# Kernel optimization log

Measured on AMD Instinct MI355X. Metric: run time of the kernel, lower is better.

## Reference

```python
import jax, jax.numpy as jnp
import numpy as np

B, H, W = 1024, 66, 64
N = 62          # EEG channels / graph nodes
TOPK = 62       # hardcoded in Network
NUM_CLASSES = 3


def setup_inputs() -> dict:
    key = jax.random.key(0)
    ks = jax.random.split(key, 17)
    p = lambda i, s: (jax.random.normal(ks[i], s, jnp.float32) * 0.05)
    return {
        "x": jax.random.normal(ks[0], (B, H, W), jnp.float32),
        "conv_w": p(1, (32, 1, 5, 5)), "conv_b": p(2, (32,)),
        "s1_bn_w": p(3, (480, 64)), "s1_bn_b": p(4, (64,)),
        "s1_g_w": p(5, (480, 32)), "s1_g_b": p(6, (32,)),
        "s2_bn_w": p(7, (32, 64)), "s2_bn_b": p(8, (64,)),
        "s2_g_w": p(9, (32, 32)), "s2_g_b": p(10, (32,)),
        "s3_bn_w": p(11, (32, 64)), "s3_bn_b": p(12, (64,)),
        "s3_g_w": p(13, (32, 32)), "s3_g_b": p(14, (32,)),
        "fc_w": p(15, (620, NUM_CLASSES)), "fc_b": p(16, (NUM_CLASSES,)),
    }


def _maxpool_last(x, k):
    # MaxPool over the last dim with kernel=stride=k, VALID (floor) semantics.
    win = (1,) * (x.ndim - 1) + (k,)
    return jax.lax.reduce_window(x, -jnp.inf, jax.lax.max, win, win, "VALID")


def _sogc(x, bn_w, bn_b, g_w, g_b):
    # x: (Bg, N, F). Self-organized graph construction + DenseGCNConv.
    Bg = x.shape[0]
    xa = jnp.tanh(x @ bn_w + bn_b)                     # (Bg, N, bn)
    adj = jax.nn.softmax(jnp.einsum("bnf,bmf->bnm", xa, xa), axis=2)
    # topk mask per row (scatter of ones at top-k column indices)
    _, idx = jax.lax.top_k(adj, TOPK)                  # (Bg, N, k)
    bi = jnp.arange(Bg)[:, None, None]
    ri = jnp.arange(N)[None, :, None]
    mask = jnp.zeros_like(adj).at[bi, ri, idx].set(1.0)
    adj = adj * mask
    # SOGC adds eye, then DenseGCNConv(add_loop=True) overwrites diag with 1
    d = jnp.arange(N)
    adj = adj.at[:, d, d].set(1.0)
    # symmetric degree normalization with clamp(min=1)
    deg_is = jnp.clip(adj.sum(-1), 1.0, None) ** -0.5  # (Bg, N)
    adj = deg_is[:, :, None] * adj * deg_is[:, None, :]
    return jnp.einsum("bnm,bmo->bno", adj, x @ g_w) + g_b


def reference(x, conv_w, conv_b, s1_bn_w, s1_bn_b, s1_g_w, s1_g_b,
              s2_bn_w, s2_bn_b, s2_g_w, s2_g_b,
              s3_bn_w, s3_bn_b, s3_g_w, s3_g_b, fc_w, fc_b):
    b = x.shape[0]
    h = jax.lax.conv_general_dilated(
        x[:, None], conv_w, (1, 1), "VALID",
        dimension_numbers=("NCHW", "OIHW", "NCHW"))
    h = jax.nn.relu(h + conv_b[None, :, None, None])   # (B,32,62,60)
    h = _maxpool_last(h, 4)                            # (B,32,62,15)
    h = h.reshape(b, -1, 480)                          # (B,62,480)
    h = _sogc(h.reshape(-1, N, 480), s1_bn_w, s1_bn_b, s1_g_w, s1_g_b)
    h = _sogc(h.reshape(-1, N, 32), s2_bn_w, s2_bn_b, s2_g_w, s2_g_b)
    h = _sogc(h.reshape(-1, N, 32), s3_bn_w, s3_bn_b, s3_g_w, s3_g_b)
    h = _maxpool_last(h, 3)                            # (B,62,10)
    h = h.reshape(h.shape[0], -1)                      # (B,620) — adapted head
    return h @ fc_w + fc_b                             # (B,3)
```

## Files before the change

### kernel.cpp

```cpp
#include <hip/hip_runtime.h>
#include <math.h>


typedef short bf16x8 __attribute__((ext_vector_type(8)));
typedef float f32x4  __attribute__((ext_vector_type(4)));
typedef float f32x16 __attribute__((ext_vector_type(16)));

__device__ __forceinline__ unsigned short f32_to_bf16_rne(float f) {
    unsigned int u = __builtin_bit_cast(unsigned int, f);
    u += 0x7fffu + ((u >> 16) & 1u);
    return (unsigned short)(u >> 16);
}
__device__ __forceinline__ float bf16_bits_to_f32(unsigned short h) {
    unsigned int u = ((unsigned int)h) << 16;
    return __builtin_bit_cast(float, u);
}
__device__ __forceinline__ float fast_tanh(float v) {
    v = fminf(fmaxf(v, -15.f), 15.f);
    const float ex = __expf(2.f * v);
    return (ex - 1.f) / (ex + 1.f);
}


__global__ __launch_bounds__(256) void prepack_kernel(
    const float* __restrict__ bnw1, const float* __restrict__ gw1,
    const float* __restrict__ cw,
    const float* __restrict__ bnw2, const float* __restrict__ gw2,
    const float* __restrict__ bnw3, const float* __restrict__ gw3,
    unsigned short* __restrict__ wp)
{
    const int idx = blockIdx.x * 256 + threadIdx.x;
    if (idx < 49152) {
        const int kc = idx / 3072, r = idx - kc * 3072;
        const int q = r / 768, r2 = r - q * 768;
        const int col = r2 >> 3, j = r2 & 7;
        float w = 0.f;
        if (kc < 15) {
            const int s = q * 8 + j;
            const int ko = s * 15 + kc;
            w = (col < 64) ? bnw1[ko * 64 + col] : gw1[ko * 32 + (col - 64)];
        }
        wp[idx] = f32_to_bf16_rne(w);
    } else if (idx >= 92160 && idx < 93696) {
        const int e = idx - 92160;
        const int c = e >> 9, l = (e >> 3) & 63, j = e & 7;
        const int ch = l & 31, dio = l >> 5;
        const int di = (c < 2) ? (2 * c + dio) : (4 + dio);
        const float w = (j < 5 && di < 5) ? cw[ch * 25 + di * 5 + j] : 0.f;
        wp[idx] = f32_to_bf16_rne(w);
    } else if (idx >= 94208 && idx < 100352) {
        const int e2 = idx - 94208;
        const int s = e2 / 3072, r = e2 - s * 3072;
        const int col = r >> 5, k = r & 31;
        const float* bnw = s ? bnw3 : bnw2;
        const float* gw  = s ? gw3  : gw2;
        const float w = (col < 64) ? bnw[k * 64 + col] : gw[k * 32 + (col - 64)];
        wp[idx] = f32_to_bf16_rne(w);
    }
}

__global__ __launch_bounds__(256, 4) void mega_kernel(
    const float* __restrict__ x,
    const float* __restrict__ cb,
    const unsigned short* __restrict__ wp,
    const float* __restrict__ bnb1,  const float* __restrict__ gb1,
    const float* __restrict__ bnb2,  const float* __restrict__ gb2,
    const float* __restrict__ bnb3,  const float* __restrict__ gb3,
    const float* __restrict__ fcw,   const float* __restrict__ fcb,
    float* __restrict__ out)
{
    __shared__ __align__(16) char lds[37632];
    unsigned short* xb   = (unsigned short*)lds;
    unsigned short* Xcol = (unsigned short*)(lds + 13056);
    unsigned short* xaH  = (unsigned short*)lds;
    unsigned short* xaL  = xaH + 4608;
    unsigned short* zB   = xaH + 9216;
    unsigned short* P    = xaH + 11520;
    unsigned short* xB   = xaH + 16128;
    float* degis = (float*)(lds + 37376);

    const int b = blockIdx.x;
    const int tid = threadIdx.x;
    const int wv = tid >> 6, ln = tid & 63;

    const float4* xg = (const float4*)(x + (size_t)b * 4224);
    for (int idx = tid; idx < 1056; idx += 256) {
        const float4 v = xg[idx];
        const int row = idx >> 4, c4 = idx & 15;
        short4 s;
        s.x = (short)f32_to_bf16_rne(v.x);
        s.y = (short)f32_to_bf16_rne(v.y);
        s.z = (short)f32_to_bf16_rne(v.z);
        s.w = (short)f32_to_bf16_rne(v.w);
        *(short4*)(xb + row * 96 + c4 * 4) = s;
    }
    for (int idx = tid; idx < 544; idx += 256) {
        const int row = idx >> 3, w = idx & 7;
        ((unsigned int*)(xb + row * 96 + 64))[w] = 0u;
    }
    if (tid < 128) {
        const int row = 66 + (tid >> 5), w = tid & 31;
        ((unsigned int*)(xb + row * 96))[w] = 0u;
    }
    if (tid < 128)
        ((unsigned int*)(Xcol + 62 * 128))[tid] = 0u;
    __syncthreads();

    const int m = ln & 15, rp = (ln >> 4) & 1, dio = ln >> 5;
    const int ch = ln & 31, hi = ln >> 5;
    bf16x8 Wc[3];
    #pragma unroll
    for (int c = 0; c < 3; ++c)
        Wc[c] = *(const bf16x8*)(wp + 92160 + c * 512 + ln * 8);
    const float cbv = cb[ch];

    const int rt = ln & 15, q = ln >> 4;
    f32x4 acc[6];
    #pragma unroll
    for (int nt = 0; nt < 6; ++nt) acc[nt] = (f32x4){0.f, 0.f, 0.f, 0.f};

    for (int pjg = 0; pjg < 4; ++pjg) {
        const int j0 = pjg * 16;
        for (int p = wv; p < 31; p += 4) {
            const int r0 = 2 * p;
            const unsigned short* base = xb + (r0 + rp + dio) * 96 + j0 + m;
            f32x16 a32;
            #pragma unroll
            for (int i = 0; i < 16; ++i) a32[i] = 0.f;
            #pragma unroll
            for (int c = 0; c < 3; ++c) {
                bf16x8 A;
                A[0] = (short)base[c * 192 + 0];
                A[1] = (short)base[c * 192 + 1];
                A[2] = (short)base[c * 192 + 2];
                A[3] = (short)base[c * 192 + 3];
                A[4] = (short)base[c * 192 + 4];
                A[5] = A[0]; A[6] = A[1]; A[7] = A[2];
                a32 = __builtin_amdgcn_mfma_f32_32x32x16_bf16(A, Wc[c], a32, 0, 0, 0);
            }
            #pragma unroll
            for (int i = 0; i < 4; ++i) {
                const int t = 2 * i + hi;
                const int rpo = t >> 2, g = t & 3;
                float v = fmaxf(fmaxf(a32[4 * i], a32[4 * i + 1]),
                                fmaxf(a32[4 * i + 2], a32[4 * i + 3])) + cbv;
                v = fmaxf(v, 0.f);
                if (!(pjg == 3 && g == 3)) {
                    const int row = r0 + rpo;
                    const int tt = ch * 62 + row;
                    const int n = tt >> 5, sf = tt & 31;
                    Xcol[n * 128 + ((g * 32 + sf) ^ ((n & 7) << 3))] =
                        f32_to_bf16_rne(v);
                }
            }
        }
        __syncthreads();
        {
            const int row = wv * 16 + rt;
            #pragma unroll
            for (int g = 0; g < 4; ++g) {
                const int kc = pjg * 4 + g;
                const bf16x8 A = *(const bf16x8*)(
                    Xcol + row * 128 + (((g * 4 + q) ^ (row & 7)) << 3));
                #pragma unroll
                for (int nt = 0; nt < 6; ++nt) {
                    const bf16x8 Bh = *(const bf16x8*)(
                        wp + kc * 3072 + q * 768 + nt * 128 + rt * 8);
                    acc[nt] = __builtin_amdgcn_mfma_f32_16x16x32_bf16(A, Bh, acc[nt], 0, 0, 0);
                }
            }
        }
        __syncthreads();
    }

    {
        const int rq = wv * 4 + q;
        #pragma unroll
        for (int nt = 0; nt < 4; ++nt) {
            const float bb = bnb1[nt * 16 + rt];
            #pragma unroll
            for (int j = 0; j < 4; ++j) {
                const int r = rq * 4 + j;
                float th = fast_tanh(acc[nt][j] + bb);
                if (r >= 62) th = 0.f;
                const unsigned short h = f32_to_bf16_rne(th);
                const unsigned short l = f32_to_bf16_rne(th - bf16_bits_to_f32(h));
                xaH[r * 72 + nt * 16 + rt] = h;
                xaL[r * 72 + nt * 16 + rt] = l;
            }
        }
        #pragma unroll
        for (int nt = 4; nt < 6; ++nt) {
            const int o = (nt - 4) * 16 + rt;
            unsigned short zv[4];
            #pragma unroll
            for (int j = 0; j < 4; ++j) {
                const int r = rq * 4 + j;
                zv[j] = (r < 62) ? f32_to_bf16_rne(acc[nt][j]) : (unsigned short)0;
            }
            *(ushort4*)(zB + o * 72 + rq * 4) =
                make_ushort4(zv[0], zv[1], zv[2], zv[3]);
        }
    }
    __syncthreads();

    const int c16 = ln & 15;
    const unsigned short* wstg = wp + 94208;

    #pragma unroll 1
    for (int st = 0; st < 3; ++st) {
        f32x4 sacc[4];
        #pragma unroll
        for (int t = 0; t < 4; ++t) sacc[t] = (f32x4){0.f, 0.f, 0.f, 0.f};
        const int arow = (wv * 16 + c16) * 72;
        #pragma unroll
        for (int kh = 0; kh < 2; ++kh) {
            const int chh = (kh * 4 + q) * 8;
            const bf16x8 AH = *(const bf16x8*)(xaH + arow + chh);
            const bf16x8 AL = *(const bf16x8*)(xaL + arow + chh);
            #pragma unroll
            for (int t = 0; t < 4; ++t) {
                const bf16x8 BH = *(const bf16x8*)(xaH + (t * 16 + c16) * 72 + chh);
                const bf16x8 BL = *(const bf16x8*)(xaL + (t * 16 + c16) * 72 + chh);
                sacc[t] = __builtin_amdgcn_mfma_f32_16x16x32_bf16(AH, BH, sacc[t], 0, 0, 0);
                sacc[t] = __builtin_amdgcn_mfma_f32_16x16x32_bf16(AH, BL, sacc[t], 0, 0, 0);
                sacc[t] = __builtin_amdgcn_mfma_f32_16x16x32_bf16(AL, BH, sacc[t], 0, 0, 0);
            }
        }
        float e[4][4], dri[4];
        #pragma unroll
        for (int j = 0; j < 4; ++j) {
            const int n = wv * 16 + q * 4 + j;
            const float v0 = sacc[0][j], v1 = sacc[1][j];
            const float v2 = sacc[2][j], v3 = sacc[3][j];
            float mx = fmaxf(fmaxf(v0, v1), v2);
            if (c16 < 14) mx = fmaxf(mx, v3);
            mx = fmaxf(mx, __shfl_xor(mx, 1));
            mx = fmaxf(mx, __shfl_xor(mx, 2));
            mx = fmaxf(mx, __shfl_xor(mx, 4));
            mx = fmaxf(mx, __shfl_xor(mx, 8));
            float e0 = __expf(v0 - mx), e1 = __expf(v1 - mx), e2 = __expf(v2 - mx);
            float e3 = (c16 < 14) ? __expf(v3 - mx) : 0.f;
            float sum = e0 + e1 + e2 + e3;
            sum += __shfl_xor(sum, 1);
            sum += __shfl_xor(sum, 2);
            sum += __shfl_xor(sum, 4);
            sum += __shfl_xor(sum, 8);
            const float inv = 1.f / sum;
            e0 *= inv; e1 *= inv; e2 *= inv; e3 *= inv;
            if (n < 62 && c16 == (n & 15)) {
                const int dt = n >> 4;
                if (dt == 0) e0 = 1.f;
                else if (dt == 1) e1 = 1.f;
                else if (dt == 2) e2 = 1.f;
                else e3 = 1.f;
            }
            float dg = e0 + e1 + e2 + e3;
            dg += __shfl_xor(dg, 1);
            dg += __shfl_xor(dg, 2);
            dg += __shfl_xor(dg, 4);
            dg += __shfl_xor(dg, 8);
            const float d = rsqrtf(fmaxf(dg, 1.f));
            if (c16 == 0) degis[n] = d;
            dri[j] = d;
            e[j][0] = e0; e[j][1] = e1; e[j][2] = e2; e[j][3] = e3;
        }
        __syncthreads();
        {
            const float dm0 = degis[c16],      dm1 = degis[16 + c16];
            const float dm2 = degis[32 + c16], dm3 = degis[48 + c16];
            #pragma unroll
            for (int j = 0; j < 4; ++j) {
                const int n = wv * 16 + q * 4 + j;
                unsigned short* pr = P + n * 72 + c16;
                if (n < 62) {
                    pr[0]  = f32_to_bf16_rne(e[j][0] * dri[j] * dm0);
                    pr[16] = f32_to_bf16_rne(e[j][1] * dri[j] * dm1);
                    pr[32] = f32_to_bf16_rne(e[j][2] * dri[j] * dm2);
                    pr[48] = f32_to_bf16_rne(e[j][3] * dri[j] * dm3);
                } else { pr[0] = 0; pr[16] = 0; pr[32] = 0; pr[48] = 0; }
            }
        }
        __syncthreads();
        {
            f32x4 oa0 = {0.f, 0.f, 0.f, 0.f}, oa1 = {0.f, 0.f, 0.f, 0.f};
            #pragma unroll
            for (int kh = 0; kh < 2; ++kh) {
                const int chh = (kh * 4 + q) * 8;
                const bf16x8 pa = *(const bf16x8*)(P + (wv * 16 + c16) * 72 + chh);
                const bf16x8 z0 = *(const bf16x8*)(zB + c16 * 72 + chh);
                const bf16x8 z1 = *(const bf16x8*)(zB + (16 + c16) * 72 + chh);
                oa0 = __builtin_amdgcn_mfma_f32_16x16x32_bf16(pa, z0, oa0, 0, 0, 0);
                oa1 = __builtin_amdgcn_mfma_f32_16x16x32_bf16(pa, z1, oa1, 0, 0, 0);
            }
            const float* gbp = (st == 0) ? gb1 : (st == 1) ? gb2 : gb3;
            const float g0 = gbp[c16], g1 = gbp[16 + c16];
            #pragma unroll
            for (int j = 0; j < 4; ++j) {
                const int n = wv * 16 + q * 4 + j;
                unsigned short* xr = xB + n * 40 + c16;
                if (n < 62) {
                    xr[0]  = f32_to_bf16_rne(oa0[j] + g0);
                    xr[16] = f32_to_bf16_rne(oa1[j] + g1);
                } else { xr[0] = 0; xr[16] = 0; }
            }
        }
        __syncthreads();
        if (st == 2) break;

        {
            const unsigned short* wsB = wstg + st * 3072;
            const float* bnbp = (st == 0) ? bnb2 : bnb3;
            const bf16x8 ax = *(const bf16x8*)(xB + (wv * 16 + c16) * 40 + q * 8);
            f32x4 sa[6];
            #pragma unroll
            for (int nt = 0; nt < 6; ++nt) {
                const bf16x8 wb = *(const bf16x8*)(wsB + (nt * 16 + c16) * 32 + q * 8);
                f32x4 zz = {0.f, 0.f, 0.f, 0.f};
                sa[nt] = __builtin_amdgcn_mfma_f32_16x16x32_bf16(ax, wb, zz, 0, 0, 0);
            }
            #pragma unroll
            for (int nt = 0; nt < 4; ++nt) {
                const float bb = bnbp[nt * 16 + c16];
                #pragma unroll
                for (int j = 0; j < 4; ++j) {
                    const int n = wv * 16 + q * 4 + j;
                    float th = fast_tanh(sa[nt][j] + bb);
                    if (n >= 62) th = 0.f;
                    const unsigned short h = f32_to_bf16_rne(th);
                    const unsigned short l = f32_to_bf16_rne(th - bf16_bits_to_f32(h));
                    xaH[n * 72 + nt * 16 + c16] = h;
                    xaL[n * 72 + nt * 16 + c16] = l;
                }
            }
            #pragma unroll
            for (int nt = 4; nt < 6; ++nt) {
                const int o = (nt - 4) * 16 + c16;
                unsigned short zv[4];
                #pragma unroll
                for (int j = 0; j < 4; ++j) {
                    const int n = wv * 16 + q * 4 + j;
                    zv[j] = (n < 62) ? f32_to_bf16_rne(sa[nt][j]) : (unsigned short)0;
                }
                *(ushort4*)(zB + o * 72 + wv * 16 + q * 4) =
                    make_ushort4(zv[0], zv[1], zv[2], zv[3]);
            }
        }
        __syncthreads();
    }

    float a0 = 0.f, a1 = 0.f, a2 = 0.f;
    for (int t = tid; t < 620; t += 256) {
        const int n = t / 10, tt = t - (t / 10) * 10;
        const unsigned short* pr = xB + n * 40 + tt * 3;
        const float p = fmaxf(fmaxf(bf16_bits_to_f32(pr[0]), bf16_bits_to_f32(pr[1])),
                              bf16_bits_to_f32(pr[2]));
        const float* fw = fcw + t * 3;
        a0 = fmaf(p, fw[0], a0);
        a1 = fmaf(p, fw[1], a1);
        a2 = fmaf(p, fw[2], a2);
    }
    #pragma unroll
    for (int off = 32; off; off >>= 1) {
        a0 += __shfl_down(a0, off);
        a1 += __shfl_down(a1, off);
        a2 += __shfl_down(a2, off);
    }
    float* red = degis;
    if (ln == 0) { red[wv * 3 + 0] = a0; red[wv * 3 + 1] = a1; red[wv * 3 + 2] = a2; }
    __syncthreads();
    if (tid == 0) {
        out[b * 3 + 0] = red[0] + red[3] + red[6] + red[9]  + fcb[0];
        out[b * 3 + 1] = red[1] + red[4] + red[7] + red[10] + fcb[1];
        out[b * 3 + 2] = red[2] + red[5] + red[8] + red[11] + fcb[2];
    }
}

extern "C" void kernel_launch(void* const* d_in, const int* in_sizes, int n_in,
                              void* d_out, int out_size, void* d_ws, size_t ws_size,
                              hipStream_t stream) {
    const float* x     = (const float*)d_in[0];
    const float* convw = (const float*)d_in[1];
    const float* convb = (const float*)d_in[2];
    const float* bnw1  = (const float*)d_in[3];
    const float* bnb1  = (const float*)d_in[4];
    const float* gw1   = (const float*)d_in[5];
    const float* gb1   = (const float*)d_in[6];
    const float* bnw2  = (const float*)d_in[7];
    const float* bnb2  = (const float*)d_in[8];
    const float* gw2   = (const float*)d_in[9];
    const float* gb2   = (const float*)d_in[10];
    const float* bnw3  = (const float*)d_in[11];
    const float* bnb3  = (const float*)d_in[12];
    const float* gw3   = (const float*)d_in[13];
    const float* gb3   = (const float*)d_in[14];
    const float* fcw   = (const float*)d_in[15];
    const float* fcb   = (const float*)d_in[16];

    unsigned short* wp = (unsigned short*)d_ws;

    prepack_kernel<<<392, 256, 0, stream>>>(bnw1, gw1, convw, bnw2, gw2,
                                            bnw3, gw3, wp);
    mega_kernel<<<1024, 256, 0, stream>>>(x, convb, wp, bnb1, gb1,
                                          bnb2, gb2, bnb3, gb3,
                                          fcw, fcb, (float*)d_out);
}
```

Before: 87.26 us.

## Switch all MFMA paths from bf16 to fp16 and drop split-precision adjacency GEMM

```diff
diff --git a/kernel.cpp b/kernel.cpp
--- a/kernel.cpp
+++ b/kernel.cpp
@@ -2,18 +2,17 @@
 #include <math.h>
 
 
-typedef short bf16x8 __attribute__((ext_vector_type(8)));
-typedef float f32x4  __attribute__((ext_vector_type(4)));
-typedef float f32x16 __attribute__((ext_vector_type(16)));
-
-__device__ __forceinline__ unsigned short f32_to_bf16_rne(float f) {
-    unsigned int u = __builtin_bit_cast(unsigned int, f);
-    u += 0x7fffu + ((u >> 16) & 1u);
-    return (unsigned short)(u >> 16);
-}
-__device__ __forceinline__ float bf16_bits_to_f32(unsigned short h) {
-    unsigned int u = ((unsigned int)h) << 16;
-    return __builtin_bit_cast(float, u);
+typedef _Float16 f16x8 __attribute__((ext_vector_type(8)));
+typedef short    s16x8 __attribute__((ext_vector_type(8)));
+typedef float    f32x4  __attribute__((ext_vector_type(4)));
+typedef float    f32x16 __attribute__((ext_vector_type(16)));
+
+__device__ __forceinline__ unsigned short f32_to_f16u(float f) {
+    const _Float16 h = (_Float16)f;
+    return __builtin_bit_cast(unsigned short, h);
+}
+__device__ __forceinline__ float f16u_to_f32(unsigned short u) {
+    return (float)__builtin_bit_cast(_Float16, u);
 }
 __device__ __forceinline__ float fast_tanh(float v) {
     v = fminf(fmaxf(v, -15.f), 15.f);
@@ -40,14 +39,14 @@
             const int ko = s * 15 + kc;
             w = (col < 64) ? bnw1[ko * 64 + col] : gw1[ko * 32 + (col - 64)];
         }
-        wp[idx] = f32_to_bf16_rne(w);
+        wp[idx] = f32_to_f16u(w);
     } else if (idx >= 92160 && idx < 93696) {
         const int e = idx - 92160;
         const int c = e >> 9, l = (e >> 3) & 63, j = e & 7;
         const int ch = l & 31, dio = l >> 5;
         const int di = (c < 2) ? (2 * c + dio) : (4 + dio);
         const float w = (j < 5 && di < 5) ? cw[ch * 25 + di * 5 + j] : 0.f;
-        wp[idx] = f32_to_bf16_rne(w);
+        wp[idx] = f32_to_f16u(w);
     } else if (idx >= 94208 && idx < 100352) {
         const int e2 = idx - 94208;
         const int s = e2 / 3072, r = e2 - s * 3072;
@@ -55,7 +54,7 @@
         const float* bnw = s ? bnw3 : bnw2;
         const float* gw  = s ? gw3  : gw2;
         const float w = (col < 64) ? bnw[k * 64 + col] : gw[k * 32 + (col - 64)];
-        wp[idx] = f32_to_bf16_rne(w);
+        wp[idx] = f32_to_f16u(w);
     }
 }
 
@@ -69,15 +68,14 @@
     const float* __restrict__ fcw,   const float* __restrict__ fcb,
     float* __restrict__ out)
 {
-    __shared__ __align__(16) char lds[37632];
+    __shared__ __align__(16) char lds[28416];
     unsigned short* xb   = (unsigned short*)lds;
-    unsigned short* Xcol = (unsigned short*)(lds + 13056);
+    unsigned short* Xcol = (unsigned short*)(lds + 10880);
     unsigned short* xaH  = (unsigned short*)lds;
-    unsigned short* xaL  = xaH + 4608;
-    unsigned short* zB   = xaH + 9216;
-    unsigned short* P    = xaH + 11520;
-    unsigned short* xB   = xaH + 16128;
-    float* degis = (float*)(lds + 37376);
+    unsigned short* zB   = xaH + 4608;
+    unsigned short* P    = xaH + 6912;
+    unsigned short* xB   = xaH + 11520;
+    float* degis = (float*)(lds + 28160);
 
     const int b = blockIdx.x;
     const int tid = threadIdx.x;
@@ -88,19 +86,19 @@
         const float4 v = xg[idx];
         const int row = idx >> 4, c4 = idx & 15;
         short4 s;
-        s.x = (short)f32_to_bf16_rne(v.x);
-        s.y = (short)f32_to_bf16_rne(v.y);
-        s.z = (short)f32_to_bf16_rne(v.z);
-        s.w = (short)f32_to_bf16_rne(v.w);
-        *(short4*)(xb + row * 96 + c4 * 4) = s;
+        s.x = (short)f32_to_f16u(v.x);
+        s.y = (short)f32_to_f16u(v.y);
+        s.z = (short)f32_to_f16u(v.z);
+        s.w = (short)f32_to_f16u(v.w);
+        *(short4*)(xb + row * 80 + c4 * 4) = s;
     }
     for (int idx = tid; idx < 544; idx += 256) {
         const int row = idx >> 3, w = idx & 7;
-        ((unsigned int*)(xb + row * 96 + 64))[w] = 0u;
-    }
-    if (tid < 128) {
+        ((unsigned int*)(xb + row * 80 + 64))[w] = 0u;
+    }
+    if (tid < 64) {
         const int row = 66 + (tid >> 5), w = tid & 31;
-        ((unsigned int*)(xb + row * 96))[w] = 0u;
+        ((unsigned int*)(xb + row * 80))[w] = 0u;
     }
     if (tid < 128)
         ((unsigned int*)(Xcol + 62 * 128))[tid] = 0u;
@@ -108,11 +106,12 @@
 
     const int m = ln & 15, rp = (ln >> 4) & 1, dio = ln >> 5;
     const int ch = ln & 31, hi = ln >> 5;
-    bf16x8 Wc[3];
+    f16x8 Wc[3];
     #pragma unroll
     for (int c = 0; c < 3; ++c)
-        Wc[c] = *(const bf16x8*)(wp + 92160 + c * 512 + ln * 8);
+        Wc[c] = *(const f16x8*)(wp + 92160 + c * 512 + ln * 8);
     const float cbv = cb[ch];
+    const f32x16 z16 = {};
 
     const int rt = ln & 15, q = ln >> 4;
     f32x4 acc[6];
@@ -123,20 +122,20 @@
         const int j0 = pjg * 16;
         for (int p = wv; p < 31; p += 4) {
             const int r0 = 2 * p;
-            const unsigned short* base = xb + (r0 + rp + dio) * 96 + j0 + m;
+            const unsigned short* base = xb + (r0 + rp + dio) * 80 + j0 + m;
             f32x16 a32;
             #pragma unroll
-            for (int i = 0; i < 16; ++i) a32[i] = 0.f;
-            #pragma unroll
             for (int c = 0; c < 3; ++c) {
-                bf16x8 A;
-                A[0] = (short)base[c * 192 + 0];
-                A[1] = (short)base[c * 192 + 1];
-                A[2] = (short)base[c * 192 + 2];
-                A[3] = (short)base[c * 192 + 3];
-                A[4] = (short)base[c * 192 + 4];
+                s16x8 A;
+                A[0] = (short)base[c * 160 + 0];
+                A[1] = (short)base[c * 160 + 1];
+                A[2] = (short)base[c * 160 + 2];
+                A[3] = (short)base[c * 160 + 3];
+                A[4] = (short)base[c * 160 + 4];
                 A[5] = A[0]; A[6] = A[1]; A[7] = A[2];
-                a32 = __builtin_amdgcn_mfma_f32_32x32x16_bf16(A, Wc[c], a32, 0, 0, 0);
+                const f16x8 Af = __builtin_bit_cast(f16x8, A);
+                a32 = __builtin_amdgcn_mfma_f32_32x32x16_f16(
+                          Af, Wc[c], (c == 0) ? z16 : a32, 0, 0, 0);
             }
             #pragma unroll
             for (int i = 0; i < 4; ++i) {
@@ -150,7 +149,7 @@
                     const int tt = ch * 62 + row;
                     const int n = tt >> 5, sf = tt & 31;
                     Xcol[n * 128 + ((g * 32 + sf) ^ ((n & 7) << 3))] =
-                        f32_to_bf16_rne(v);
+                        f32_to_f16u(v);
                 }
             }
         }
@@ -160,13 +159,13 @@
             #pragma unroll
             for (int g = 0; g < 4; ++g) {
                 const int kc = pjg * 4 + g;
-                const bf16x8 A = *(const bf16x8*)(
+                const f16x8 A = *(const f16x8*)(
                     Xcol + row * 128 + (((g * 4 + q) ^ (row & 7)) << 3));
                 #pragma unroll
                 for (int nt = 0; nt < 6; ++nt) {
-                    const bf16x8 Bh = *(const bf16x8*)(
+                    const f16x8 Bh = *(const f16x8*)(
                         wp + kc * 3072 + q * 768 + nt * 128 + rt * 8);
-                    acc[nt] = __builtin_amdgcn_mfma_f32_16x16x32_bf16(A, Bh, acc[nt], 0, 0, 0);
+                    acc[nt] = __builtin_amdgcn_mfma_f32_16x16x32_f16(A, Bh, acc[nt], 0, 0, 0);
                 }
             }
         }
@@ -183,10 +182,7 @@
                 const int r = rq * 4 + j;
                 float th = fast_tanh(acc[nt][j] + bb);
                 if (r >= 62) th = 0.f;
-                const unsigned short h = f32_to_bf16_rne(th);
-                const unsigned short l = f32_to_bf16_rne(th - bf16_bits_to_f32(h));
-                xaH[r * 72 + nt * 16 + rt] = h;
-                xaL[r * 72 + nt * 16 + rt] = l;
+                xaH[r * 72 + nt * 16 + rt] = f32_to_f16u(th);
             }
         }
         #pragma unroll
@@ -196,7 +192,7 @@
             #pragma unroll
             for (int j = 0; j < 4; ++j) {
                 const int r = rq * 4 + j;
-                zv[j] = (r < 62) ? f32_to_bf16_rne(acc[nt][j]) : (unsigned short)0;
+                zv[j] = (r < 62) ? f32_to_f16u(acc[nt][j]) : (unsigned short)0;
             }
             *(ushort4*)(zB + o * 72 + rq * 4) =
                 make_ushort4(zv[0], zv[1], zv[2], zv[3]);
@@ -216,15 +212,11 @@
         #pragma unroll
         for (int kh = 0; kh < 2; ++kh) {
             const int chh = (kh * 4 + q) * 8;
-            const bf16x8 AH = *(const bf16x8*)(xaH + arow + chh);
-            const bf16x8 AL = *(const bf16x8*)(xaL + arow + chh);
+            const f16x8 AH = *(const f16x8*)(xaH + arow + chh);
             #pragma unroll
             for (int t = 0; t < 4; ++t) {
-                const bf16x8 BH = *(const bf16x8*)(xaH + (t * 16 + c16) * 72 + chh);
-                const bf16x8 BL = *(const bf16x8*)(xaL + (t * 16 + c16) * 72 + chh);
-                sacc[t] = __builtin_amdgcn_mfma_f32_16x16x32_bf16(AH, BH, sacc[t], 0, 0, 0);
-                sacc[t] = __builtin_amdgcn_mfma_f32_16x16x32_bf16(AH, BL, sacc[t], 0, 0, 0);
-                sacc[t] = __builtin_amdgcn_mfma_f32_16x16x32_bf16(AL, BH, sacc[t], 0, 0, 0);
+                const f16x8 BH = *(const f16x8*)(xaH + (t * 16 + c16) * 72 + chh);
+                sacc[t] = __builtin_amdgcn_mfma_f32_16x16x32_f16(AH, BH, sacc[t], 0, 0, 0);
             }
         }
         float e[4][4], dri[4];
@@ -274,10 +266,10 @@
                 const int n = wv * 16 + q * 4 + j;
                 unsigned short* pr = P + n * 72 + c16;
                 if (n < 62) {
-                    pr[0]  = f32_to_bf16_rne(e[j][0] * dri[j] * dm0);
-                    pr[16] = f32_to_bf16_rne(e[j][1] * dri[j] * dm1);
-                    pr[32] = f32_to_bf16_rne(e[j][2] * dri[j] * dm2);
-                    pr[48] = f32_to_bf16_rne(e[j][3] * dri[j] * dm3);
+                    pr[0]  = f32_to_f16u(e[j][0] * dri[j] * dm0);
+                    pr[16] = f32_to_f16u(e[j][1] * dri[j] * dm1);
+                    pr[32] = f32_to_f16u(e[j][2] * dri[j] * dm2);
+                    pr[48] = f32_to_f16u(e[j][3] * dri[j] * dm3);
                 } else { pr[0] = 0; pr[16] = 0; pr[32] = 0; pr[48] = 0; }
             }
         }
@@ -287,11 +279,11 @@
             #pragma unroll
             for (int kh = 0; kh < 2; ++kh) {
                 const int chh = (kh * 4 + q) * 8;
-                const bf16x8 pa = *(const bf16x8*)(P + (wv * 16 + c16) * 72 + chh);
-                const bf16x8 z0 = *(const bf16x8*)(zB + c16 * 72 + chh);
-                const bf16x8 z1 = *(const bf16x8*)(zB + (16 + c16) * 72 + chh);
-                oa0 = __builtin_amdgcn_mfma_f32_16x16x32_bf16(pa, z0, oa0, 0, 0, 0);
-                oa1 = __builtin_amdgcn_mfma_f32_16x16x32_bf16(pa, z1, oa1, 0, 0, 0);
+                const f16x8 pa = *(const f16x8*)(P + (wv * 16 + c16) * 72 + chh);
+                const f16x8 z0 = *(const f16x8*)(zB + c16 * 72 + chh);
+                const f16x8 z1 = *(const f16x8*)(zB + (16 + c16) * 72 + chh);
+                oa0 = __builtin_amdgcn_mfma_f32_16x16x32_f16(pa, z0, oa0, 0, 0, 0);
+                oa1 = __builtin_amdgcn_mfma_f32_16x16x32_f16(pa, z1, oa1, 0, 0, 0);
             }
             const float* gbp = (st == 0) ? gb1 : (st == 1) ? gb2 : gb3;
             const float g0 = gbp[c16], g1 = gbp[16 + c16];
@@ -300,8 +292,8 @@
                 const int n = wv * 16 + q * 4 + j;
                 unsigned short* xr = xB + n * 40 + c16;
                 if (n < 62) {
-                    xr[0]  = f32_to_bf16_rne(oa0[j] + g0);
-                    xr[16] = f32_to_bf16_rne(oa1[j] + g1);
+                    xr[0]  = f32_to_f16u(oa0[j] + g0);
+                    xr[16] = f32_to_f16u(oa1[j] + g1);
                 } else { xr[0] = 0; xr[16] = 0; }
             }
         }
@@ -311,13 +303,13 @@
         {
             const unsigned short* wsB = wstg + st * 3072;
             const float* bnbp = (st == 0) ? bnb2 : bnb3;
-            const bf16x8 ax = *(const bf16x8*)(xB + (wv * 16 + c16) * 40 + q * 8);
+            const f16x8 ax = *(const f16x8*)(xB + (wv * 16 + c16) * 40 + q * 8);
             f32x4 sa[6];
             #pragma unroll
             for (int nt = 0; nt < 6; ++nt) {
-                const bf16x8 wb = *(const bf16x8*)(wsB + (nt * 16 + c16) * 32 + q * 8);
+                const f16x8 wb = *(const f16x8*)(wsB + (nt * 16 + c16) * 32 + q * 8);
                 f32x4 zz = {0.f, 0.f, 0.f, 0.f};
-                sa[nt] = __builtin_amdgcn_mfma_f32_16x16x32_bf16(ax, wb, zz, 0, 0, 0);
+                sa[nt] = __builtin_amdgcn_mfma_f32_16x16x32_f16(ax, wb, zz, 0, 0, 0);
             }
             #pragma unroll
             for (int nt = 0; nt < 4; ++nt) {
@@ -327,10 +319,7 @@
                     const int n = wv * 16 + q * 4 + j;
                     float th = fast_tanh(sa[nt][j] + bb);
                     if (n >= 62) th = 0.f;
-                    const unsigned short h = f32_to_bf16_rne(th);
-                    const unsigned short l = f32_to_bf16_rne(th - bf16_bits_to_f32(h));
-                    xaH[n * 72 + nt * 16 + c16] = h;
-                    xaL[n * 72 + nt * 16 + c16] = l;
+                    xaH[n * 72 + nt * 16 + c16] = f32_to_f16u(th);
                 }
             }
             #pragma unroll
@@ -340,7 +329,7 @@
                 #pragma unroll
                 for (int j = 0; j < 4; ++j) {
                     const int n = wv * 16 + q * 4 + j;
-                    zv[j] = (n < 62) ? f32_to_bf16_rne(sa[nt][j]) : (unsigned short)0;
+                    zv[j] = (n < 62) ? f32_to_f16u(sa[nt][j]) : (unsigned short)0;
                 }
                 *(ushort4*)(zB + o * 72 + wv * 16 + q * 4) =
                     make_ushort4(zv[0], zv[1], zv[2], zv[3]);
@@ -353,8 +342,8 @@
     for (int t = tid; t < 620; t += 256) {
         const int n = t / 10, tt = t - (t / 10) * 10;
         const unsigned short* pr = xB + n * 40 + tt * 3;
-        const float p = fmaxf(fmaxf(bf16_bits_to_f32(pr[0]), bf16_bits_to_f32(pr[1])),
-                              bf16_bits_to_f32(pr[2]));
+        const float p = fmaxf(fmaxf(f16u_to_f32(pr[0]), f16u_to_f32(pr[1])),
+                              f16u_to_f32(pr[2]));
         const float* fw = fcw + t * 3;
         a0 = fmaf(p, fw[0], a0);
         a1 = fmaf(p, fw[1], a1);
```

Measured after the change: 83.64 us. 4.1% less time.
